# Performance work log

Measured on AMD Instinct MI355X. Metric: run time of the kernel, lower is better.

Reference implementation:

```python
import jax, jax.numpy as jnp
import numpy as np

N, NC, E, S = 65536, 24576, 524288, 256
VAR_DIM, H1, H2, H3, H4 = 6, 128, 128, 256, 128
THRE, EPS = 0.7, 1e-5


def _bn(x, g, b):
    # BatchNorm1d, training-mode batch statistics (biased var), dropout treated as identity
    mu = x.mean(0)
    v = x.var(0)
    return (x - mu) * jax.lax.rsqrt(v + EPS) * g + b


def _gcn_sparse(h, src, dst, ew, W, b):
    # PyG GCNConv with edge weights: add self-loops (weight 1), symmetric normalization
    n = h.shape[0]
    loop = jnp.arange(n)
    s = jnp.concatenate([src, loop])
    d = jnp.concatenate([dst, loop])
    w = jnp.concatenate([ew, jnp.ones((n,), h.dtype)])
    deg = jax.ops.segment_sum(w, d, num_segments=n)
    dinv = jnp.where(deg > 0, jax.lax.rsqrt(deg), 0.0)
    norm = dinv[s] * w * dinv[d]
    xw = h @ W.T  # [n, out]
    out = jax.ops.segment_sum(norm[:, None] * xw[s], d, num_segments=n)
    return out + b


def _gcn_dense(h, A, W, b):
    # GCNConv on a dense binary adjacency (no edge weights), self-loops + sym norm
    n = h.shape[0]
    A_hat = A + jnp.eye(n, dtype=h.dtype)
    deg = A_hat.sum(0)
    dinv = jnp.where(deg > 0, jax.lax.rsqrt(deg), 0.0)
    return dinv[:, None] * (A_hat.T @ ((h @ W.T) * dinv[:, None])) + b


def setup_inputs() -> dict:
    key = jax.random.key(0)
    ks = jax.random.split(key, 10)

    def w(k, o, i):
        return jax.random.normal(k, (o, i), jnp.float32) / np.float32(np.sqrt(i))

    x = jax.random.normal(ks[0], (N, VAR_DIM), jnp.float32)
    edge_attr = jax.random.uniform(ks[1], (E,), jnp.float32)
    scen_adj = jax.random.uniform(ks[2], (S, S), jnp.float32)
    edge_index = jax.random.randint(ks[3], (2, E), 0, N)
    batch = jnp.arange(N) // (N // S)  # sorted node->graph ids, 256 nodes per graph
    mark = jnp.concatenate([jnp.ones((NC,), jnp.int32), jnp.zeros((N - NC,), jnp.int32)])
    return {
        "x": x, "edge_attr": edge_attr, "scen_adj": scen_adj,
        "mlp_var_w": w(ks[4], H1, VAR_DIM), "mlp_var_b": jnp.zeros((H1,), jnp.float32),
        "mlp_con_w": w(ks[5], H1, 1), "mlp_con_b": jnp.zeros((H1,), jnp.float32),
        "conv1_w": w(ks[6], H2, H1), "conv1_b": jnp.zeros((H2,), jnp.float32),
        "conv2_w": w(ks[7], H3, H2), "conv2_b": jnp.zeros((H3,), jnp.float32),
        "conv3_w": w(ks[8], H4, H3), "conv3_b": jnp.zeros((H4,), jnp.float32),
        "bn1_g": jnp.ones((H1,), jnp.float32), "bn1_b": jnp.zeros((H1,), jnp.float32),
        "bn2_g": jnp.ones((H2,), jnp.float32), "bn2_b": jnp.zeros((H2,), jnp.float32),
        "bn3_g": jnp.ones((H3,), jnp.float32), "bn3_b": jnp.zeros((H3,), jnp.float32),
        "mark": mark, "edge_index": edge_index, "batch": batch, "n_con": NC,
    }


def reference(x, edge_attr, scen_adj, mlp_var_w, mlp_var_b, mlp_con_w, mlp_con_b,
              conv1_w, conv1_b, conv2_w, conv2_b, conv3_w, conv3_b,
              bn1_g, bn1_b, bn2_g, bn2_b, bn3_g, bn3_b,
              mark, edge_index, batch, n_con):
    nc = int(n_con)  # mark layout: first nc nodes are constraints (mark==1), rest vars
    con_feat = jnp.tanh(x[:nc, 0:1] @ mlp_con_w.T + mlp_con_b)
    var_feat = jnp.tanh(x[nc:] @ mlp_var_w.T + mlp_var_b)
    h = jnp.concatenate([con_feat, var_feat], axis=0)  # [N, H1], con-first as in torch cat
    h = _bn(h, bn1_g, bn1_b)  # dropout = identity (eval)
    h = _gcn_sparse(h, edge_index[0], edge_index[1], edge_attr, conv1_w, conv1_b)
    h = jnp.tanh(_bn(h, bn2_g, bn2_b))
    s = scen_adj.shape[0]
    sums = jax.ops.segment_sum(h, batch, num_segments=s)
    cnt = jax.ops.segment_sum(jnp.ones((h.shape[0],), h.dtype), batch, num_segments=s)
    pooled = sums / jnp.maximum(cnt, 1.0)[:, None]  # global_mean_pool -> [S, H2]
    A = (scen_adj >= THRE).astype(h.dtype)  # filter_adj + unweighted edges
    f = jnp.tanh(_bn(_gcn_dense(pooled, A, conv2_w, conv2_b), bn3_g, bn3_b))
    feat = jnp.tanh(_gcn_dense(f, A, conv3_w, conv3_b))
    return feat, feat.mean(0)
```

## Files before the change

kernel.cpp:

```cpp
#include <hip/hip_runtime.h>
#include <hip/hip_bf16.h>
#include <cstddef>

#define N_NODES 65536
#define N_EDGES 524288
#define S_GRAPH 256
#define BN_EPS 1e-5f
#define THRE 0.7f

typedef __hip_bfloat16 bf16;
typedef unsigned int uint32;
typedef unsigned char uchar;
typedef unsigned short ushort16;
typedef __attribute__((ext_vector_type(8))) short short8;
typedef __attribute__((ext_vector_type(4))) float f32x4;

__device__ __forceinline__ float blo(uint32 u) { return __uint_as_float(u << 16); }
__device__ __forceinline__ float bhi(uint32 u) { return __uint_as_float(u & 0xffff0000u); }

__device__ __forceinline__ uint32 packbf(float a, float b)
{
    bf16 ha = __float2bfloat16(a), hb = __float2bfloat16(b);
    unsigned short ua, ub;
    __builtin_memcpy(&ua, &ha, 2); __builtin_memcpy(&ub, &hb, 2);
    return (uint32)ua | ((uint32)ub << 16);
}

__device__ __forceinline__ float ftanh(float x)
{
    float e = __builtin_amdgcn_exp2f(x * 2.8853900817779268f);
    return 1.0f - 2.0f * __builtin_amdgcn_rcpf(e + 1.0f);
}

__global__ __launch_bounds__(256) void k_mlp_hist(
    const float* __restrict__ x, const float* __restrict__ wv,
    const float* __restrict__ bv, const float* __restrict__ wc,
    const float* __restrict__ bc, const int* __restrict__ nconp,
    uint32* __restrict__ h0u, float* __restrict__ pstat,
    const int* __restrict__ dst, uint32* __restrict__ blkhist,
    const float* __restrict__ scen, float* __restrict__ fcol,
    const float* __restrict__ w1f, uint32* __restrict__ w1bk,
    float* __restrict__ zacc, int* __restrict__ ctrs)
{
    __shared__ float xs[128 * 6];
    __shared__ float sh[256];
    __shared__ uint32 bh[256];
    int t = threadIdx.x;
    int b = blockIdx.x;
    if (b < 512) {
        bh[t] = 0;
        __syncthreads();
        int e0 = b * 1024 + t * 4;
        int4 d4 = *(const int4*)(dst + e0);
        atomicAdd(&bh[d4.x >> 8], 1u);
        atomicAdd(&bh[d4.y >> 8], 1u);
        atomicAdd(&bh[d4.z >> 8], 1u);
        atomicAdd(&bh[d4.w >> 8], 1u);
        __syncthreads();
        blkhist[b * 256 + t] = bh[t];
        return;
    }
    if (b >= 1024) {
        if (b == 1024) {
            float s = 0.f;
            for (int r = 0; r < 256; r++)
                s += (scen[r * 256 + t] >= THRE) ? 1.0f : 0.0f;
            fcol[t] = s;
        } else if (b == 1056) {
            const float4* w4 = (const float4*)w1f;
            uint2* wo = (uint2*)w1bk;
            #pragma unroll
            for (int it = 0; it < 16; it++) {
                int fi = it * 256 + t;
                float4 w = w4[fi];
                wo[fi] = make_uint2(packbf(w.x, w.y), packbf(w.z, w.w));
            }
            for (int i = t; i < 7168; i += 256) zacc[i] = 0.f;
            if (t < 8) ctrs[t] = 0;
        }
        return;
    }
    int n0 = (b - 512) * 128;
    if (t < 192) ((float4*)xs)[t] = ((const float4*)(x + (size_t)n0 * 6))[t];
    __syncthreads();

    int nc = *nconp;
    int lane = t & 63, wave = t >> 6;
    int j0 = 2 * lane;
    const float2* wv2 = (const float2*)wv;
    float2 wa0 = wv2[j0 * 3], wa1 = wv2[j0 * 3 + 1], wa2 = wv2[j0 * 3 + 2];
    float2 wb0 = wv2[j0 * 3 + 3], wb1 = wv2[j0 * 3 + 4], wb2 = wv2[j0 * 3 + 5];
    float wc0 = wc[j0], wc1 = wc[j0 + 1], bc0 = bc[j0], bc1 = bc[j0 + 1];
    float bv0 = bv[j0], bv1 = bv[j0 + 1];

    float s0 = 0.f, ss0 = 0.f, s1 = 0.f, ss1 = 0.f;
    #pragma unroll 4
    for (int m = 0; m < 32; m++) {
        int ln = wave * 32 + m;
        int n = n0 + ln;
        const float* xr = &xs[ln * 6];
        float a0, a1;
        if (n < nc) {
            float xv = xr[0];
            a0 = xv * wc0 + bc0; a1 = xv * wc1 + bc1;
        } else {
            float x0 = xr[0], x1 = xr[1], x2 = xr[2], x3 = xr[3], x4 = xr[4], x5 = xr[5];
            a0 = bv0 + x0 * wa0.x + x1 * wa0.y + x2 * wa1.x + x3 * wa1.y + x4 * wa2.x + x5 * wa2.y;
            a1 = bv1 + x0 * wb0.x + x1 * wb0.y + x2 * wb1.x + x3 * wb1.y + x4 * wb2.x + x5 * wb2.y;
        }
        uint32 pk = packbf(ftanh(a0), ftanh(a1));
        h0u[(size_t)n * 64 + lane] = pk;
        float v0 = blo(pk), v1 = bhi(pk);
        s0 += v0; ss0 += v0 * v0; s1 += v1; ss1 += v1 * v1;
    }
    float* pst = pstat + (size_t)(b - 512) * 256;
    sh[t] = s0; __syncthreads();
    if (t < 64) pst[2 * t] = sh[t] + sh[t + 64] + sh[t + 128] + sh[t + 192];
    __syncthreads(); sh[t] = s1; __syncthreads();
    if (t < 64) pst[2 * t + 1] = sh[t] + sh[t + 64] + sh[t + 128] + sh[t + 192];
    __syncthreads(); sh[t] = ss0; __syncthreads();
    if (t < 64) pst[128 + 2 * t] = sh[t] + sh[t + 64] + sh[t + 128] + sh[t + 192];
    __syncthreads(); sh[t] = ss1; __syncthreads();
    if (t < 64) pst[128 + 2 * t + 1] = sh[t] + sh[t + 64] + sh[t + 128] + sh[t + 192];
}

__global__ __launch_bounds__(256) void k_binscan(
    const uint32* __restrict__ blkhist, uint32* __restrict__ blkoff,
    uint32* __restrict__ binsz, uint32* __restrict__ ubase,
    uint32* __restrict__ pbase, const float* __restrict__ pstat,
    float* __restrict__ stats, int* __restrict__ ctr)
{
    __shared__ uint32 v[512];
    __shared__ uint32 ps[256];
    __shared__ int flag;
    int g = blockIdx.x, t = threadIdx.x;
    if (g == 256) {
        float acc = 0.f;
        for (int j = 0; j < 512; j++) acc += pstat[j * 256 + t];
        stats[t] = acc;
        return;
    }
    v[t]       = blkhist[t * 256 + g];
    v[t + 256] = blkhist[(t + 256) * 256 + g];
    __syncthreads();
    uint32 a0 = v[2 * t], a1 = v[2 * t + 1];
    ps[t] = a0 + a1; __syncthreads();
    for (int o = 1; o < 256; o <<= 1) {
        uint32 u = (t >= o) ? ps[t - o] : 0;
        __syncthreads();
        ps[t] += u;
        __syncthreads();
    }
    uint32 ex = ps[t] - (a0 + a1);
    ((uint2*)blkoff)[g * 256 + t] = make_uint2(ex, ex + a0);
    if (t == 255) atomicExch((int*)&binsz[g], (int)ps[255]);
    __syncthreads();
    if (t == 0) {
        __threadfence();
        flag = (atomicAdd(ctr, 1) == 255) ? 1 : 0;
    }
    __syncthreads();
    if (flag) {
        __threadfence();
        uint32 s = binsz[t];
        ps[t] = s; __syncthreads();
        for (int o = 1; o < 256; o <<= 1) {
            uint32 u = (t >= o) ? ps[t - o] : 0;
            __syncthreads();
            ps[t] += u;
            __syncthreads();
        }
        ubase[t] = ps[t] - s;
        pbase[t] = ps[t] - s + (uint32)t * 768u;
    }
}

__global__ __launch_bounds__(256) void k_sg(
    const int* __restrict__ src, const int* __restrict__ dst,
    const float* __restrict__ ew, const uint32* __restrict__ blkoff,
    const uint32* __restrict__ ubase, uint2* __restrict__ ebin,
    const uint32* __restrict__ h0u, const uint32* __restrict__ w1bk,
    const float* __restrict__ g1, const float* __restrict__ bb1,
    const float* __restrict__ stats, ushort16* __restrict__ xws)
{
    __shared__ __align__(16) uchar smem[53248];
    int t = threadIdx.x, b = blockIdx.x;
    if (b < 512) {
        uint32* bh = (uint32*)smem;
        uint32* bo = (uint32*)(smem + 1024);
        bh[t] = 0;
        bo[t] = ubase[t] + blkoff[t * 512 + b];
        __syncthreads();
        int e0 = b * 1024 + t * 4;
        int4 d4 = *(const int4*)(dst + e0);
        int4 s4 = *(const int4*)(src + e0);
        float4 w4 = *(const float4*)(ew + e0);
        int bin; uint32 r;
        bin = d4.x >> 8; r = atomicAdd(&bh[bin], 1u);
        ebin[bo[bin] + r] = make_uint2((uint32)s4.x | ((uint32)(d4.x & 255) << 16), __float_as_uint(w4.x));
        bin = d4.y >> 8; r = atomicAdd(&bh[bin], 1u);
        ebin[bo[bin] + r] = make_uint2((uint32)s4.y | ((uint32)(d4.y & 255) << 16), __float_as_uint(w4.y));
        bin = d4.z >> 8; r = atomicAdd(&bh[bin], 1u);
        ebin[bo[bin] + r] = make_uint2((uint32)s4.z | ((uint32)(d4.z & 255) << 16), __float_as_uint(w4.z));
        bin = d4.w >> 8; r = atomicAdd(&bh[bin], 1u);
        ebin[bo[bin] + r] = make_uint2((uint32)s4.w | ((uint32)(d4.w & 255) << 16), __float_as_uint(w4.w));
        return;
    }
    short* hn_s = (short*)smem;
    short* w_s  = (short*)(smem + 17408);
    float* sc   = (float*)(smem + 52224);
    float* sf   = (float*)(smem + 52736);
    int row0 = (b - 512) * 64;

    if (t < 128) {
        float mu  = stats[t] * (1.0f / N_NODES);
        float var = stats[128 + t] * (1.0f / N_NODES) - mu * mu;
        float rs  = rsqrtf(fmaxf(var, 0.f) + BN_EPS);
        float s   = rs * g1[t];
        sc[t] = s;
        sf[t] = bb1[t] - mu * s;
    }
    __syncthreads();

    const uint4* h4 = (const uint4*)(h0u + (size_t)row0 * 64);
    #pragma unroll
    for (int it = 0; it < 4; it++) {
        int slot = it * 256 + t;
        int r = slot >> 4, k0 = (slot & 15) * 8;
        uint4 u = h4[slot];
        uint32 ua[4] = {u.x, u.y, u.z, u.w};
        uint32 o[4];
        #pragma unroll
        for (int m = 0; m < 4; m++) {
            int k = k0 + 2 * m;
            o[m] = packbf(blo(ua[m]) * sc[k] + sf[k], bhi(ua[m]) * sc[k + 1] + sf[k + 1]);
        }
        *(uint4*)&hn_s[r * 136 + k0] = make_uint4(o[0], o[1], o[2], o[3]);
    }
    const uint4* wv4 = (const uint4*)w1bk;
    #pragma unroll
    for (int it = 0; it < 8; it++) {
        int s2 = it * 256 + t;
        int c = s2 >> 4, k0 = (s2 & 15) * 8;
        *(uint4*)&w_s[c * 136 + k0] = wv4[s2];
    }
    __syncthreads();

    int lane = t & 63, wave = t >> 6;
    int m16 = lane & 15, kh = lane >> 4;
    int mbase = wave * 16;
    f32x4 acc[8] = {};
    #pragma unroll
    for (int ks = 0; ks < 4; ks++) {
        short8 a = *(const short8*)&hn_s[(mbase + m16) * 136 + ks * 32 + kh * 8];
        #pragma unroll
        for (int ct = 0; ct < 8; ct++) {
            short8 bfr = *(const short8*)&w_s[(ct * 16 + m16) * 136 + ks * 32 + kh * 8];
            acc[ct] = __builtin_amdgcn_mfma_f32_16x16x32_bf16(a, bfr, acc[ct], 0, 0, 0);
        }
    }
    #pragma unroll
    for (int ct = 0; ct < 8; ct++) {
        int col = ct * 16 + m16;
        #pragma unroll
        for (int r = 0; r < 4; r++) {
            int row = mbase + kh * 4 + r;
            bf16 hv = __float2bfloat16(acc[ct][r]);
            unsigned short us; __builtin_memcpy(&us, &hv, 2);
            xws[(size_t)(row0 + row) * 128 + col] = us;
        }
    }
}

__global__ __launch_bounds__(256) void k_csr(
    const uint2* __restrict__ ebin, const uint32* __restrict__ binsz,
    const uint32* __restrict__ ubase, const uint32* __restrict__ pbase,
    float* __restrict__ dinv, int* __restrict__ rowp, int* __restrict__ cnts,
    int2* __restrict__ epk, uint32* __restrict__ xwu)
{
    __shared__ uint2 es[3072];
    __shared__ uint32 hist[256];
    __shared__ int sscan[256];
    __shared__ int rloc[256];
    __shared__ float dlv[256];
    int g = blockIdx.x, t = threadIdx.x;
    int start = (int)ubase[g];
    int sz = min((int)binsz[g], 3072);
    int pb = (int)pbase[g];
    hist[t] = 0;
    __syncthreads();
    for (int i = t; i < sz; i += 256) {
        uint2 e = ebin[start + i];
        int dl = (e.x >> 16) & 255;
        uint32 wfix = __float2uint_rn(__uint_as_float(e.y) * 262144.0f);
        uint32 h = atomicAdd(&hist[dl], (1u << 24) | wfix);
        e.x |= (h >> 24) << 24;
        es[i] = e;
    }
    __syncthreads();
    uint32 hv = hist[t];
    int cnt = (int)(hv >> 24);
    float di = rsqrtf((float)(hv & 0xFFFFFFu) * 3.814697265625e-6f + 1.0f);
    dlv[t] = di;
    dinv[g * 256 + t] = di;
    cnts[g * 256 + t] = cnt;
    int pcnt = (cnt + 3) & ~3;
    sscan[t] = pcnt; __syncthreads();
    for (int o = 1; o < 256; o <<= 1) {
        int u = (t >= o) ? sscan[t - o] : 0;
        __syncthreads();
        sscan[t] += u;
        __syncthreads();
    }
    int rl = sscan[t] - pcnt;
    rloc[t] = rl;
    rowp[g * 256 + t] = pb + rl;
    __syncthreads();
    for (int i = t; i < sz; i += 256) {
        uint2 e = es[i];
        int s  = (int)(e.x & 0xFFFFu);
        int dl = (int)((e.x >> 16) & 255u);
        int r  = (int)(e.x >> 24);
        float w = __uint_as_float(e.y) * dlv[dl];
        epk[pb + rloc[dl] + r] = make_int2(s, __float_as_int(w));
    }
    int base = pb + rl;
    for (int q = cnt; q < pcnt; q++) epk[base + q] = make_int2(g * 256 + t, 0);
    uint4* xr = (uint4*)(xwu + (size_t)g * 256 * 64);
    for (int i = t; i < 4096; i += 256) {
        float d = dlv[i >> 4];
        uint4 u = xr[i];
        u.x = packbf(blo(u.x) * d, bhi(u.x) * d);
        u.y = packbf(blo(u.y) * d, bhi(u.y) * d);
        u.z = packbf(blo(u.z) * d, bhi(u.z) * d);
        u.w = packbf(blo(u.w) * d, bhi(u.w) * d);
        xr[i] = u;
    }
}

__global__ __launch_bounds__(256) void k_gather(
    const int* __restrict__ rowp, const int* __restrict__ cnts,
    const int2* __restrict__ epk, const uint32* __restrict__ xwu,
    const float* __restrict__ dinv, const float2* __restrict__ b1c2,
    uint32* __restrict__ aggu, float* __restrict__ stats2r)
{
    __shared__ float sh[256];
    int t = threadIdx.x, b = blockIdx.x;
    int lane = t & 63, wave = t >> 6;
    float2 bb = b1c2[lane];
    float s0 = 0.f, ss0 = 0.f, s1 = 0.f, ss1 = 0.f;
    for (int it = 0; it < 8; it++) {
        int n = b * 32 + it * 4 + wave;
        int st = rowp[n];
        int pcnt = (cnts[n] + 3) & ~3;
        float di = dinv[n];
        uint32 u0 = xwu[(size_t)n * 64 + lane];
        float ax = di * blo(u0) + bb.x;
        float ay = di * bhi(u0) + bb.y;
        int en = st + pcnt;
        int p = st;
        for (; p + 8 <= en; p += 8) {
            int2 q0 = epk[p],     q1 = epk[p + 1], q2 = epk[p + 2], q3 = epk[p + 3];
            int2 q4 = epk[p + 4], q5 = epk[p + 5], q6 = epk[p + 6], q7 = epk[p + 7];
            uint32 v0 = xwu[(size_t)q0.x * 64 + lane];
            uint32 v1 = xwu[(size_t)q1.x * 64 + lane];
            uint32 v2 = xwu[(size_t)q2.x * 64 + lane];
            uint32 v3 = xwu[(size_t)q3.x * 64 + lane];
            uint32 v4 = xwu[(size_t)q4.x * 64 + lane];
            uint32 v5 = xwu[(size_t)q5.x * 64 + lane];
            uint32 v6 = xwu[(size_t)q6.x * 64 + lane];
            uint32 v7 = xwu[(size_t)q7.x * 64 + lane];
            float w0 = __int_as_float(q0.y), w1 = __int_as_float(q1.y);
            float w2 = __int_as_float(q2.y), w3 = __int_as_float(q3.y);
            float w4 = __int_as_float(q4.y), w5 = __int_as_float(q5.y);
            float w6 = __int_as_float(q6.y), w7 = __int_as_float(q7.y);
            ax += w0 * blo(v0) + w1 * blo(v1) + w2 * blo(v2) + w3 * blo(v3);
            ay += w0 * bhi(v0) + w1 * bhi(v1) + w2 * bhi(v2) + w3 * bhi(v3);
            ax += w4 * blo(v4) + w5 * blo(v5) + w6 * blo(v6) + w7 * blo(v7);
            ay += w4 * bhi(v4) + w5 * bhi(v5) + w6 * bhi(v6) + w7 * bhi(v7);
        }
        if (p < en) {
            int2 q0 = epk[p], q1 = epk[p + 1], q2 = epk[p + 2], q3 = epk[p + 3];
            uint32 v0 = xwu[(size_t)q0.x * 64 + lane];
            uint32 v1 = xwu[(size_t)q1.x * 64 + lane];
            uint32 v2 = xwu[(size_t)q2.x * 64 + lane];
            uint32 v3 = xwu[(size_t)q3.x * 64 + lane];
            float w0 = __int_as_float(q0.y), w1 = __int_as_float(q1.y);
            float w2 = __int_as_float(q2.y), w3 = __int_as_float(q3.y);
            ax += w0 * blo(v0) + w1 * blo(v1) + w2 * blo(v2) + w3 * blo(v3);
            ay += w0 * bhi(v0) + w1 * bhi(v1) + w2 * bhi(v2) + w3 * bhi(v3);
        }
        uint32 pk = packbf(ax, ay);
        aggu[(size_t)n * 64 + lane] = pk;
        float v0 = blo(pk), v1 = bhi(pk);
        s0 += v0; ss0 += v0 * v0; s1 += v1; ss1 += v1 * v1;
    }
    float* st2 = stats2r + (b & 7) * 256;
    sh[t] = s0; __syncthreads();
    if (t < 64) atomicAdd(&st2[2 * t], sh[t] + sh[t + 64] + sh[t + 128] + sh[t + 192]);
    __syncthreads(); sh[t] = s1; __syncthreads();
    if (t < 64) atomicAdd(&st2[2 * t + 1], sh[t] + sh[t + 64] + sh[t + 128] + sh[t + 192]);
    __syncthreads(); sh[t] = ss0; __syncthreads();
    if (t < 64) atomicAdd(&st2[128 + 2 * t], sh[t] + sh[t + 64] + sh[t + 128] + sh[t + 192]);
    __syncthreads(); sh[t] = ss1; __syncthreads();
    if (t < 64) atomicAdd(&st2[128 + 2 * t + 1], sh[t] + sh[t + 64] + sh[t + 128] + sh[t + 192]);
}

__global__ __launch_bounds__(512) void k_poolg2(
    const uint32* __restrict__ aggu, const float* __restrict__ stats2r,
    const float* __restrict__ g2, const float* __restrict__ bb2,
    const float* __restrict__ w2, float* __restrict__ z1)
{
    __shared__ float sc[128], sf[128], sh[512], prow[128];
    int t = threadIdx.x, g = blockIdx.x;
    if (t < 128) {
        float su = 0.f, sq = 0.f;
        #pragma unroll
        for (int r = 0; r < 8; r++) {
            su += stats2r[r * 256 + t];
            sq += stats2r[r * 256 + 128 + t];
        }
        float mu  = su * (1.0f / N_NODES);
        float var = sq * (1.0f / N_NODES) - mu * mu;
        float rs  = rsqrtf(fmaxf(var, 0.f) + BN_EPS);
        float s   = rs * g2[t];
        sc[t] = s;
        sf[t] = bb2[t] - mu * s;
    }
    __syncthreads();
    int c = t & 63, grp = t >> 6;
    float c0s = sc[2 * c], c0f = sf[2 * c], c1s = sc[2 * c + 1], c1f = sf[2 * c + 1];
    const uint32* base = aggu + (size_t)g * 256 * 64;
    float s0 = 0.f, s1 = 0.f;
    for (int r = grp * 32; r < grp * 32 + 32; r++) {
        uint32 u = base[r * 64 + c];
        s0 += ftanh(blo(u) * c0s + c0f);
        s1 += ftanh(bhi(u) * c1s + c1f);
    }
    sh[t] = s0; __syncthreads();
    if (t < 64) {
        float acc = 0.f;
        #pragma unroll
        for (int k = 0; k < 8; k++) acc += sh[t + 64 * k];
        prow[2 * t] = acc * (1.0f / 256.0f);
    }
    __syncthreads(); sh[t] = s1; __syncthreads();
    if (t < 64) {
        float acc = 0.f;
        #pragma unroll
        for (int k = 0; k < 8; k++) acc += sh[t + 64 * k];
        prow[2 * t + 1] = acc * (1.0f / 256.0f);
    }
    __syncthreads();
    if (t < 256) {
        float acc = 0.f;
        const float* wr = w2 + t * 128;
        for (int k = 0; k < 128; k++) acc += prow[k] * wr[k];
        z1[g * 256 + t] = acc;
    }
}

__global__ void k_dgcn1(const float* __restrict__ scen, const float* __restrict__ fcol,
                        const float* __restrict__ z1, const float* __restrict__ b2c,
                        float* __restrict__ y1, float* __restrict__ stats3r)
{
    __shared__ float wk[256];
    int i = blockIdx.x, t = threadIdx.x;
    float a = (scen[t * 256 + i] >= THRE) ? 1.0f : 0.0f;
    if (t == i) a += 1.0f;
    wk[t] = a * rsqrtf(fcol[t] + 1.0f);
    __syncthreads();
    float acc = 0.f;
    for (int k = 0; k < 256; k++) acc += wk[k] * z1[k * 256 + t];
    float v = rsqrtf(fcol[i] + 1.0f) * acc + b2c[t];
    y1[i * 256 + t] = v;
    float* s3 = stats3r + (i & 7) * 512;
    atomicAdd(&s3[t], v);
    atomicAdd(&s3[256 + t], v * v);
}

__global__ void k_gemm3(const float* __restrict__ y1, const float* __restrict__ stats3r,
                        const float* __restrict__ g3, const float* __restrict__ bb3,
                        const float* __restrict__ w3, float* __restrict__ z2)
{
    __shared__ float row[256];
    int i = blockIdx.x, t = threadIdx.x;
    for (int c = t; c < 256; c += 128) {
        float s = 0.f, ss = 0.f;
        #pragma unroll
        for (int r = 0; r < 8; r++) {
            s  += stats3r[r * 512 + c];
            ss += stats3r[r * 512 + 256 + c];
        }
        float mu  = s * (1.0f / 256.0f);
        float var = ss * (1.0f / 256.0f) - mu * mu;
        float rs  = rsqrtf(fmaxf(var, 0.f) + BN_EPS);
        float scj = rs * g3[c];
        float sfj = bb3[c] - mu * scj;
        row[c] = ftanh(y1[i * 256 + c] * scj + sfj);
    }
    __syncthreads();
    float acc = 0.f;
    const float* wr = w3 + t * 256;
    for (int k = 0; k < 256; k++) acc += row[k] * wr[k];
    z2[i * 128 + t] = acc;
}

__global__ void k_dgcn2(const float* __restrict__ scen, const float* __restrict__ fcol,
                        const float* __restrict__ z2, const float* __restrict__ b3c,
                        float* __restrict__ out, float* __restrict__ meanr,
                        int* __restrict__ ctr)
{
    __shared__ float wk[256];
    __shared__ int flag;
    int i = blockIdx.x, t = threadIdx.x;
    for (int k = t; k < 256; k += 128) {
        float a = (scen[k * 256 + i] >= THRE) ? 1.0f : 0.0f;
        if (k == i) a += 1.0f;
        wk[k] = a * rsqrtf(fcol[k] + 1.0f);
    }
    __syncthreads();
    float acc = 0.f;
    for (int k = 0; k < 256; k++) acc += wk[k] * z2[k * 128 + t];
    float v = ftanh(rsqrtf(fcol[i] + 1.0f) * acc + b3c[t]);
    out[i * 128 + t] = v;
    atomicAdd(&meanr[(i & 7) * 128 + t], v);
    __syncthreads();
    if (t == 0) {
        __threadfence();
        flag = (atomicAdd(ctr, 1) == 255) ? 1 : 0;
    }
    __syncthreads();
    if (flag) {
        __threadfence();
        float s = 0.f;
        #pragma unroll
        for (int r = 0; r < 8; r++) s += meanr[r * 128 + t];
        out[S_GRAPH * 128 + t] = s * (1.0f / 256.0f);
    }
}

extern "C" void kernel_launch(void* const* d_in, const int* in_sizes, int n_in,
                              void* d_out, int out_size, void* d_ws, size_t ws_size,
                              hipStream_t stream)
{
    const float* x        = (const float*)d_in[0];
    const float* edge_attr= (const float*)d_in[1];
    const float* scen     = (const float*)d_in[2];
    const float* wv       = (const float*)d_in[3];
    const float* bv       = (const float*)d_in[4];
    const float* wc       = (const float*)d_in[5];
    const float* bc       = (const float*)d_in[6];
    const float* w1       = (const float*)d_in[7];
    const float* b1c      = (const float*)d_in[8];
    const float* w2       = (const float*)d_in[9];
    const float* b2c      = (const float*)d_in[10];
    const float* w3       = (const float*)d_in[11];
    const float* b3c      = (const float*)d_in[12];
    const float* g1       = (const float*)d_in[13];
    const float* bb1      = (const float*)d_in[14];
    const float* g2       = (const float*)d_in[15];
    const float* bb2      = (const float*)d_in[16];
    const float* g3       = (const float*)d_in[17];
    const float* bb3      = (const float*)d_in[18];
    const int*  ei        = (const int*)d_in[20];
    const int*  nconp     = (const int*)d_in[22];
    const int*  src = ei;
    const int*  dst = ei + N_EDGES;

    float* wsf = (float*)d_ws;
    uint32*   h0u  = (uint32*)wsf;
    uint32*   aggu = (uint32*)wsf;
    uint32*   xwu  = (uint32*)(wsf + 4194304);
    float* zb      = wsf + 8388608;
    float* stats1  = zb;
    float* zacc    = zb + 512;
    float* stats2r = zacc;
    float* stats3r = zacc + 2048;
    float* meanr   = zacc + 6144;
    float* fcol    = zb + 7680;
    int*   ctrs    = (int*)(zb + 7936);
    float* deg     = zb + 7944;
    int*   rowp    = (int*)(deg + 65536);
    int*   cnts    = rowp + 65536;
    uint32* blkhist= (uint32*)(cnts + 65536);
    uint32* blkoff = blkhist + 131072;
    uint32* binsz  = blkoff + 131072;
    uint32* ubase  = binsz + 256;
    uint32* pbase  = ubase + 256;
    uint2* ebin    = (uint2*)(pbase + 256);
    int2*  epk     = (int2*)(ebin + 524288);
    uint32* w1bk   = (uint32*)(epk + 720896);
    float* z1      = (float*)(w1bk + 8192);
    float* y1      = z1 + 65536;
    float* z2      = y1 + 65536;
    float* pstat   = z2 + 32768;

    float* out = (float*)d_out;

    k_mlp_hist<<<1057, 256, 0, stream>>>(x, wv, bv, wc, bc, nconp, h0u, pstat,
                                         dst, blkhist, scen, fcol, w1, w1bk,
                                         zacc, ctrs);
    k_binscan<<<257, 256, 0, stream>>>(blkhist, blkoff, binsz, ubase, pbase,
                                       pstat, stats1, &ctrs[0]);
    k_sg<<<1536, 256, 0, stream>>>(src, dst, edge_attr, blkoff, ubase, ebin,
                                   h0u, w1bk, g1, bb1, stats1, (ushort16*)xwu);
    k_csr<<<256, 256, 0, stream>>>(ebin, binsz, ubase, pbase, deg, rowp, cnts,
                                   epk, xwu);
    k_gather<<<2048, 256, 0, stream>>>(rowp, cnts, epk, xwu, deg,
                                       (const float2*)b1c, aggu, stats2r);
    k_poolg2<<<S_GRAPH, 512, 0, stream>>>(aggu, stats2r, g2, bb2, w2, z1);
    k_dgcn1<<<256, 256, 0, stream>>>(scen, fcol, z1, b2c, y1, stats3r);
    k_gemm3<<<256, 128, 0, stream>>>(y1, stats3r, g3, bb3, w3, z2);
    k_dgcn2<<<256, 128, 0, stream>>>(scen, fcol, z2, b3c, out, meanr, &ctrs[1]);
}
```

Measured before the change: 237.9 us.

## Apply source dinv in gather instead of rescaling xw, split-K small dense kernels

The pass in k_csr that rescales the whole bf16 xw matrix by the source degree normalisation is removed. k_gather now multiplies each edge weight by dinv of the source node and uses dinv squared for the self-loop term. This drops a full read-modify-write of the 16 MB feature matrix and one bf16 rounding, at the cost of an extra random 4-byte load per edge. Separately, k_gemm3 and k_dgcn2 go from 128 to 256 threads with a two-way split over the reduction dimension and a shared-memory combine.

```diff
diff --git a/kernel.cpp b/kernel.cpp
--- a/kernel.cpp
+++ b/kernel.cpp
@@ -276,7 +276,7 @@
     const uint2* __restrict__ ebin, const uint32* __restrict__ binsz,
     const uint32* __restrict__ ubase, const uint32* __restrict__ pbase,
     float* __restrict__ dinv, int* __restrict__ rowp, int* __restrict__ cnts,
-    int2* __restrict__ epk, uint32* __restrict__ xwu)
+    int2* __restrict__ epk)
 {
     __shared__ uint2 es[3072];
     __shared__ uint32 hist[256];
@@ -326,16 +326,6 @@
     }
     int base = pb + rl;
     for (int q = cnt; q < pcnt; q++) epk[base + q] = make_int2(g * 256 + t, 0);
-    uint4* xr = (uint4*)(xwu + (size_t)g * 256 * 64);
-    for (int i = t; i < 4096; i += 256) {
-        float d = dlv[i >> 4];
-        uint4 u = xr[i];
-        u.x = packbf(blo(u.x) * d, bhi(u.x) * d);
-        u.y = packbf(blo(u.y) * d, bhi(u.y) * d);
-        u.z = packbf(blo(u.z) * d, bhi(u.z) * d);
-        u.w = packbf(blo(u.w) * d, bhi(u.w) * d);
-        xr[i] = u;
-    }
 }
 
 __global__ __launch_bounds__(256) void k_gather(
@@ -354,9 +344,10 @@
         int st = rowp[n];
         int pcnt = (cnts[n] + 3) & ~3;
         float di = dinv[n];
+        float d2 = di * di;
         uint32 u0 = xwu[(size_t)n * 64 + lane];
-        float ax = di * blo(u0) + bb.x;
-        float ay = di * bhi(u0) + bb.y;
+        float ax = d2 * blo(u0) + bb.x;
+        float ay = d2 * bhi(u0) + bb.y;
         int en = st + pcnt;
         int p = st;
         for (; p + 8 <= en; p += 8) {
@@ -370,10 +361,14 @@
             uint32 v5 = xwu[(size_t)q5.x * 64 + lane];
             uint32 v6 = xwu[(size_t)q6.x * 64 + lane];
             uint32 v7 = xwu[(size_t)q7.x * 64 + lane];
-            float w0 = __int_as_float(q0.y), w1 = __int_as_float(q1.y);
-            float w2 = __int_as_float(q2.y), w3 = __int_as_float(q3.y);
-            float w4 = __int_as_float(q4.y), w5 = __int_as_float(q5.y);
-            float w6 = __int_as_float(q6.y), w7 = __int_as_float(q7.y);
+            float w0 = __int_as_float(q0.y) * dinv[q0.x];
+            float w1 = __int_as_float(q1.y) * dinv[q1.x];
+            float w2 = __int_as_float(q2.y) * dinv[q2.x];
+            float w3 = __int_as_float(q3.y) * dinv[q3.x];
+            float w4 = __int_as_float(q4.y) * dinv[q4.x];
+            float w5 = __int_as_float(q5.y) * dinv[q5.x];
+            float w6 = __int_as_float(q6.y) * dinv[q6.x];
+            float w7 = __int_as_float(q7.y) * dinv[q7.x];
             ax += w0 * blo(v0) + w1 * blo(v1) + w2 * blo(v2) + w3 * blo(v3);
             ay += w0 * bhi(v0) + w1 * bhi(v1) + w2 * bhi(v2) + w3 * bhi(v3);
             ax += w4 * blo(v4) + w5 * blo(v5) + w6 * blo(v6) + w7 * blo(v7);
@@ -385,8 +380,10 @@
             uint32 v1 = xwu[(size_t)q1.x * 64 + lane];
             uint32 v2 = xwu[(size_t)q2.x * 64 + lane];
             uint32 v3 = xwu[(size_t)q3.x * 64 + lane];
-            float w0 = __int_as_float(q0.y), w1 = __int_as_float(q1.y);
-            float w2 = __int_as_float(q2.y), w3 = __int_as_float(q3.y);
+            float w0 = __int_as_float(q0.y) * dinv[q0.x];
+            float w1 = __int_as_float(q1.y) * dinv[q1.x];
+            float w2 = __int_as_float(q2.y) * dinv[q2.x];
+            float w3 = __int_as_float(q3.y) * dinv[q3.x];
             ax += w0 * blo(v0) + w1 * blo(v1) + w2 * blo(v2) + w3 * blo(v3);
             ay += w0 * bhi(v0) + w1 * bhi(v1) + w2 * bhi(v2) + w3 * bhi(v3);
         }
@@ -479,52 +476,67 @@
     atomicAdd(&s3[256 + t], v * v);
 }
 
-__global__ void k_gemm3(const float* __restrict__ y1, const float* __restrict__ stats3r,
-                        const float* __restrict__ g3, const float* __restrict__ bb3,
-                        const float* __restrict__ w3, float* __restrict__ z2)
+__global__ __launch_bounds__(256) void k_gemm3(
+    const float* __restrict__ y1, const float* __restrict__ stats3r,
+    const float* __restrict__ g3, const float* __restrict__ bb3,
+    const float* __restrict__ w3, float* __restrict__ z2)
 {
     __shared__ float row[256];
+    __shared__ float psum[256];
     int i = blockIdx.x, t = threadIdx.x;
-    for (int c = t; c < 256; c += 128) {
+    {
         float s = 0.f, ss = 0.f;
         #pragma unroll
         for (int r = 0; r < 8; r++) {
-            s  += stats3r[r * 512 + c];
-            ss += stats3r[r * 512 + 256 + c];
+            s  += stats3r[r * 512 + t];
+            ss += stats3r[r * 512 + 256 + t];
         }
         float mu  = s * (1.0f / 256.0f);
         float var = ss * (1.0f / 256.0f) - mu * mu;
         float rs  = rsqrtf(fmaxf(var, 0.f) + BN_EPS);
-        float scj = rs * g3[c];
-        float sfj = bb3[c] - mu * scj;
-        row[c] = ftanh(y1[i * 256 + c] * scj + sfj);
-    }
-    __syncthreads();
+        float scj = rs * g3[t];
+        float sfj = bb3[t] - mu * scj;
+        row[t] = ftanh(y1[i * 256 + t] * scj + sfj);
+    }
+    __syncthreads();
+    int c = t & 127, h = t >> 7;
+    const float* wr = w3 + c * 256 + h * 128;
+    const float* rr = row + h * 128;
     float acc = 0.f;
-    const float* wr = w3 + t * 256;
-    for (int k = 0; k < 256; k++) acc += row[k] * wr[k];
-    z2[i * 128 + t] = acc;
-}
-
-__global__ void k_dgcn2(const float* __restrict__ scen, const float* __restrict__ fcol,
-                        const float* __restrict__ z2, const float* __restrict__ b3c,
-                        float* __restrict__ out, float* __restrict__ meanr,
-                        int* __restrict__ ctr)
+    for (int k = 0; k < 128; k++) acc += rr[k] * wr[k];
+    psum[t] = acc;
+    __syncthreads();
+    if (t < 128) z2[i * 128 + t] = psum[t] + psum[t + 128];
+}
+
+__global__ __launch_bounds__(256) void k_dgcn2(
+    const float* __restrict__ scen, const float* __restrict__ fcol,
+    const float* __restrict__ z2, const float* __restrict__ b3c,
+    float* __restrict__ out, float* __restrict__ meanr,
+    int* __restrict__ ctr)
 {
     __shared__ float wk[256];
+    __shared__ float psum[256];
     __shared__ int flag;
     int i = blockIdx.x, t = threadIdx.x;
-    for (int k = t; k < 256; k += 128) {
-        float a = (scen[k * 256 + i] >= THRE) ? 1.0f : 0.0f;
-        if (k == i) a += 1.0f;
-        wk[k] = a * rsqrtf(fcol[k] + 1.0f);
-    }
-    __syncthreads();
+    {
+        float a = (scen[t * 256 + i] >= THRE) ? 1.0f : 0.0f;
+        if (t == i) a += 1.0f;
+        wk[t] = a * rsqrtf(fcol[t] + 1.0f);
+    }
+    __syncthreads();
+    int c = t & 127, h = t >> 7;
+    const float* wkh = wk + h * 128;
+    const float* zc  = z2 + (size_t)h * 128 * 128 + c;
     float acc = 0.f;
-    for (int k = 0; k < 256; k++) acc += wk[k] * z2[k * 128 + t];
-    float v = ftanh(rsqrtf(fcol[i] + 1.0f) * acc + b3c[t]);
-    out[i * 128 + t] = v;
-    atomicAdd(&meanr[(i & 7) * 128 + t], v);
+    for (int k = 0; k < 128; k++) acc += wkh[k] * zc[k * 128];
+    psum[t] = acc;
+    __syncthreads();
+    if (t < 128) {
+        float v = ftanh(rsqrtf(fcol[i] + 1.0f) * (psum[t] + psum[t + 128]) + b3c[t]);
+        out[i * 128 + t] = v;
+        atomicAdd(&meanr[(i & 7) * 128 + t], v);
+    }
     __syncthreads();
     if (t == 0) {
         __threadfence();
@@ -533,10 +545,12 @@
     __syncthreads();
     if (flag) {
         __threadfence();
-        float s = 0.f;
-        #pragma unroll
-        for (int r = 0; r < 8; r++) s += meanr[r * 128 + t];
-        out[S_GRAPH * 128 + t] = s * (1.0f / 256.0f);
+        if (t < 128) {
+            float s = 0.f;
+            #pragma unroll
+            for (int r = 0; r < 8; r++) s += meanr[r * 128 + t];
+            out[S_GRAPH * 128 + t] = s * (1.0f / 256.0f);
+        }
     }
 }
 
@@ -605,12 +619,11 @@
                                        pstat, stats1, &ctrs[0]);
     k_sg<<<1536, 256, 0, stream>>>(src, dst, edge_attr, blkoff, ubase, ebin,
                                    h0u, w1bk, g1, bb1, stats1, (ushort16*)xwu);
-    k_csr<<<256, 256, 0, stream>>>(ebin, binsz, ubase, pbase, deg, rowp, cnts,
-                                   epk, xwu);
+    k_csr<<<256, 256, 0, stream>>>(ebin, binsz, ubase, pbase, deg, rowp, cnts, epk);
     k_gather<<<2048, 256, 0, stream>>>(rowp, cnts, epk, xwu, deg,
                                        (const float2*)b1c, aggu, stats2r);
     k_poolg2<<<S_GRAPH, 512, 0, stream>>>(aggu, stats2r, g2, bb2, w2, z1);
     k_dgcn1<<<256, 256, 0, stream>>>(scen, fcol, z1, b2c, y1, stats3r);
-    k_gemm3<<<256, 128, 0, stream>>>(y1, stats3r, g3, bb3, w3, z2);
-    k_dgcn2<<<256, 128, 0, stream>>>(scen, fcol, z2, b3c, out, meanr, &ctrs[1]);
-}
+    k_gemm3<<<256, 256, 0, stream>>>(y1, stats3r, g3, bb3, w3, z2);
+    k_dgcn2<<<256, 256, 0, stream>>>(scen, fcol, z2, b3c, out, meanr, &ctrs[1]);
+}
```

Result: no change. 236.5 us (-0.6%).
